# Kernel optimization log

Measured on AMD Instinct MI355X. Metric: run time of the kernel, lower is better.

## Reference

```python
import jax, jax.numpy as jnp
import numpy as np

C = 64   # in_planes
F = 40   # n_freq
T = 512  # n_frame
B = 16


def setup_inputs() -> dict:
    key = jax.random.key(0)
    kx, kq, kk, kv = jax.random.split(key, 4)
    x = jax.random.normal(kx, (B, C, F, T), dtype=jnp.float32)
    # 1x1 conv weights, no bias: [out_ch, in_ch]
    s = 1.0 / np.sqrt(C)
    Wq = jax.random.uniform(kq, (C, C), dtype=jnp.float32, minval=-s, maxval=s)
    Wk = jax.random.uniform(kk, (C, C), dtype=jnp.float32, minval=-s, maxval=s)
    Wv = jax.random.uniform(kv, (C, C), dtype=jnp.float32, minval=-s, maxval=s)
    return {"x": x, "Wq": Wq, "Wk": Wk, "Wv": Wv}


def _proj_tokens(W, x):
    # 1x1 conv (channel mix) then permute(0,3,2,1) + view -> [B, T, F*C]
    y = jnp.einsum('oc,bcft->btfo', W, x)      # [B, T, F, C]
    b, t, f, c = y.shape
    return y.reshape(b, t, f * c)


def reference(x, Wq, Wk, Wv):
    n_batch, n_planes, n_freq, n_frame = x.shape
    d = n_freq * n_planes
    q = _proj_tokens(Wq, x)                     # [B, T, d]
    k = _proj_tokens(Wk, x)
    v = _proj_tokens(Wv, x)
    scores = jnp.einsum('bqd,bkd->bqk', q, k) / jnp.sqrt(jnp.float32(d))
    attn = jax.nn.softmax(scores, axis=-1)      # [B, T, T]
    out = jnp.einsum('bqk,bkd->bqd', attn, v)   # [B, T, d]
    out = out.reshape(n_batch, n_frame, n_freq, n_planes)
    return jnp.transpose(out, (0, 3, 2, 1))     # [B, C, F, T]
```

## Files before the change

### kernel.cpp

```cpp
#include <hip/hip_runtime.h>

constexpr int B_ = 16, C_ = 64, F_ = 40, T_ = 512;
constexpr int D_ = F_ * C_;
constexpr float SCALE = 0.019764235376052372f;

typedef __attribute__((ext_vector_type(8))) short s16x8;
typedef __attribute__((ext_vector_type(4))) short s16x4;
typedef __attribute__((ext_vector_type(4))) float f32x4;

static __device__ __forceinline__ short f2bf(float f) {
  union { float f; unsigned u; } v; v.f = f;
  unsigned r = v.u + 0x7fffu + ((v.u >> 16) & 1u);
  return (short)(r >> 16);
}

static __device__ __forceinline__ f32x4 mfma16(s16x8 a, s16x8 b, f32x4 c) {
  return __builtin_amdgcn_mfma_f32_16x16x32_bf16(a, b, c, 0, 0, 0);
}

static __device__ __forceinline__ void gl2lds16(const short* g, short* l) {
  __builtin_amdgcn_global_load_lds(
      (const __attribute__((address_space(1))) unsigned int*)g,
      (__attribute__((address_space(3))) unsigned int*)l, 16, 0, 0);
}

__global__ __launch_bounds__(256) void wcvt_kernel(
    const float* __restrict__ Wq, const float* __restrict__ Wk,
    const float* __restrict__ Wv, short* __restrict__ Wb,
    float* __restrict__ rowsum)
{
  const int n = blockIdx.x * 256 + threadIdx.x;
  const int p = n >> 9;
  const int r = n & 511;
  const int mi = r >> 7;
  const int ks = (r >> 6) & 1;
  const int lane = r & 63;
  const int o = mi * 16 + (lane & 15);
  const int cb = ks * 32 + (lane >> 4) * 8;
  const float* src = (p == 0) ? Wq : (p == 1) ? Wk : Wv;
  const float sc = (p == 0) ? SCALE : 1.0f;
  const float4 a = *(const float4*)(src + o * 64 + cb);
  const float4 b2 = *(const float4*)(src + o * 64 + cb + 4);
  s16x8 s;
  s[0] = f2bf(a.x * sc);  s[1] = f2bf(a.y * sc);
  s[2] = f2bf(a.z * sc);  s[3] = f2bf(a.w * sc);
  s[4] = f2bf(b2.x * sc); s[5] = f2bf(b2.y * sc);
  s[6] = f2bf(b2.z * sc); s[7] = f2bf(b2.w * sc);
  *(s16x8*)&Wb[n * 8] = s;

  for (int i = n; i < B_ * T_; i += 6 * 256) rowsum[i] = 0.0f;
}

__global__ __launch_bounds__(256, 2) void proj_kernel(
    const float* __restrict__ x, const short* __restrict__ Wb,
    short* __restrict__ Q, short* __restrict__ K, short* __restrict__ V)
{
  constexpr int XS = 132;
  __shared__ __align__(16) short Xl[64 * XS];
  char* Ost = (char*)Xl;

  const int b = blockIdx.z, f = blockIdx.y, tt = blockIdx.x;
  const int tid = threadIdx.x;

  const float* xp = x + (((size_t)b * 64) * 40 + f) * 512 + tt * 128;
  #pragma unroll
  for (int it = 0; it < 8; ++it) {
    const int i = tid + it * 256;
    const int c = i >> 5, j = i & 31;
    const float4 v4 = *(const float4*)(xp + (size_t)c * (F_ * T_) + j * 4);
    s16x4 s4; s4[0] = f2bf(v4.x); s4[1] = f2bf(v4.y);
    s4[2] = f2bf(v4.z); s4[3] = f2bf(v4.w);
    *(s16x4*)&Xl[c * XS + j * 4] = s4;
  }
  __syncthreads();

  const int w = tid >> 6, lane = tid & 63;
  const int quad = lane >> 4, c16 = lane & 15;
  const int tl = w * 32;

  s16x8 bfrag[2][2];
  #pragma unroll
  for (int ni = 0; ni < 2; ++ni)
    #pragma unroll
    for (int ks = 0; ks < 2; ++ks) {
      const int t = tl + ni * 16 + c16;
      const int cb = ks * 32 + quad * 8;
      s16x8 tmp;
      #pragma unroll
      for (int j = 0; j < 8; ++j) tmp[j] = Xl[(cb + j) * XS + t];
      bfrag[ni][ks] = tmp;
    }
  __syncthreads();

  #pragma unroll
  for (int p = 0; p < 3; ++p) {
    s16x8 wfrag[4][2];
    #pragma unroll
    for (int mi = 0; mi < 4; ++mi)
      #pragma unroll
      for (int ks = 0; ks < 2; ++ks)
        wfrag[mi][ks] = *(const s16x8*)(Wb + ((p * 8 + mi * 2 + ks) * 64 + lane) * 8);

    if (p < 2) {
      f32x4 acc[4][2] = {};
      #pragma unroll
      for (int ks = 0; ks < 2; ++ks)
        #pragma unroll
        for (int mi = 0; mi < 4; ++mi)
          #pragma unroll
          for (int ni = 0; ni < 2; ++ni)
            acc[mi][ni] = mfma16(wfrag[mi][ks], bfrag[ni][ks], acc[mi][ni]);
      __syncthreads();
      #pragma unroll
      for (int mi = 0; mi < 4; ++mi)
        #pragma unroll
        for (int ni = 0; ni < 2; ++ni) {
          const int trow = tl + ni * 16 + c16;
          unsigned addr = trow * 128 + (mi * 32 + quad * 8);
          addr ^= (unsigned)((trow & 7) << 4);
          s16x4 s4;
          #pragma unroll
          for (int r = 0; r < 4; ++r) s4[r] = f2bf(acc[mi][ni][r]);
          *(s16x4*)(Ost + addr) = s4;
        }
      __syncthreads();
      short* outp = (p == 0) ? Q : K;
      #pragma unroll
      for (int pass = 0; pass < 4; ++pass) {
        const int row = pass * 32 + (tid >> 3);
        const int s16off = tid & 7;
        unsigned a2 = row * 128 + s16off * 16;
        a2 ^= (unsigned)((row & 7) << 4);
        const s16x8 vz = *(const s16x8*)(Ost + a2);
        *(s16x8*)&outp[(size_t)(b * 512 + tt * 128 + row) * D_ + f * 64 + s16off * 8] = vz;
      }
    } else {
      f32x4 acc[2][4] = {};
      #pragma unroll
      for (int ks = 0; ks < 2; ++ks)
        #pragma unroll
        for (int ni = 0; ni < 2; ++ni)
          #pragma unroll
          for (int mi = 0; mi < 4; ++mi)
            acc[ni][mi] = mfma16(bfrag[ni][ks], wfrag[mi][ks], acc[ni][mi]);
      __syncthreads();
      #pragma unroll
      for (int ni = 0; ni < 2; ++ni)
        #pragma unroll
        for (int mi = 0; mi < 4; ++mi) {
          const int orow = mi * 16 + c16;
          unsigned addr = orow * 256 + (tl + ni * 16 + quad * 4) * 2;
          addr ^= (unsigned)((orow & 7) << 4);
          s16x4 s4;
          #pragma unroll
          for (int r = 0; r < 4; ++r) s4[r] = f2bf(acc[ni][mi][r]);
          *(s16x4*)(Ost + addr) = s4;
        }
      __syncthreads();
      #pragma unroll
      for (int pass = 0; pass < 4; ++pass) {
        const int row = pass * 16 + (tid >> 4);
        const int s16off = tid & 15;
        unsigned a2 = row * 256 + s16off * 16;
        a2 ^= (unsigned)((row & 7) << 4);
        const s16x8 vz = *(const s16x8*)(Ost + a2);
        *(s16x8*)&V[((size_t)(b * D_ + f * 64 + row)) * 512 + tt * 128 + s16off * 8] = vz;
      }
    }
    if (p < 2) __syncthreads();
  }
}

__global__ __launch_bounds__(256) void scores_kernel(
    const short* __restrict__ Q, const short* __restrict__ K,
    short* __restrict__ A, float* __restrict__ rowsum)
{
  __shared__ __align__(16) short As[64 * 64];
  __shared__ __align__(16) short Bs[128 * 64];
  const int b = blockIdx.y;
  const int mt = blockIdx.x >> 2, nt = blockIdx.x & 3;
  const int m0 = mt * 64, n0 = nt * 128;
  const int tid = threadIdx.x;
  const int w = tid >> 6, lane = tid & 63, quad = lane >> 4, c16 = lane & 15;
  const int wm = (w >> 1) * 32, wn = (w & 1) * 64;

  const short* qb = Q + (size_t)(b * 512 + m0) * D_;
  const short* kb = K + (size_t)(b * 512 + n0) * D_;

  const short* agp[2];
  short* aldsb[2];
  #pragma unroll
  for (int i = 0; i < 2; ++i) {
    const int s = i * 256 + tid, row = s >> 3;
    const int g = (s & 7) ^ (row & 7);
    agp[i] = qb + (size_t)row * D_ + g * 8;
    aldsb[i] = &As[(i * 256 + w * 64) * 8];
  }
  const short* bgp[4];
  short* bldsb[4];
  #pragma unroll
  for (int i = 0; i < 4; ++i) {
    const int s = i * 256 + tid, row = s >> 3;
    const int g = (s & 7) ^ (row & 7);
    bgp[i] = kb + (size_t)row * D_ + g * 8;
    bldsb[i] = &Bs[(i * 256 + w * 64) * 8];
  }

  const short* amp[2][2];
  #pragma unroll
  for (int mi = 0; mi < 2; ++mi)
    #pragma unroll
    for (int ks = 0; ks < 2; ++ks) {
      const int row = wm + mi * 16 + c16;
      const int g = (ks * 4 + quad) ^ (row & 7);
      amp[mi][ks] = &As[row * 64 + g * 8];
    }
  const short* bmp[4][2];
  #pragma unroll
  for (int ni = 0; ni < 4; ++ni)
    #pragma unroll
    for (int ks = 0; ks < 2; ++ks) {
      const int row = wn + ni * 16 + c16;
      const int g = (ks * 4 + quad) ^ (row & 7);
      bmp[ni][ks] = &Bs[row * 64 + g * 8];
    }

  f32x4 acc[2][4] = {};
  constexpr int NK = D_ / 64;
  for (int kk = 0; kk < NK; ++kk) {
    const int ko = kk * 64;
    __syncthreads();
    #pragma unroll
    for (int i = 0; i < 2; ++i) gl2lds16(agp[i] + ko, aldsb[i]);
    #pragma unroll
    for (int i = 0; i < 4; ++i) gl2lds16(bgp[i] + ko, bldsb[i]);
    __syncthreads();
    s16x8 am[2][2], bm[4][2];
    #pragma unroll
    for (int mi = 0; mi < 2; ++mi)
      #pragma unroll
      for (int ks = 0; ks < 2; ++ks) am[mi][ks] = *(const s16x8*)amp[mi][ks];
    #pragma unroll
    for (int ni = 0; ni < 4; ++ni)
      #pragma unroll
      for (int ks = 0; ks < 2; ++ks) bm[ni][ks] = *(const s16x8*)bmp[ni][ks];
    #pragma unroll
    for (int ks = 0; ks < 2; ++ks)
      #pragma unroll
      for (int mi = 0; mi < 2; ++mi)
        #pragma unroll
        for (int ni = 0; ni < 4; ++ni)
          acc[mi][ni] = mfma16(am[mi][ks], bm[ni][ks], acc[mi][ni]);
  }

  float* rsb = rowsum + b * 512;
  #pragma unroll
  for (int mi = 0; mi < 2; ++mi)
    #pragma unroll
    for (int r = 0; r < 4; ++r) {
      float part = 0.f;
      #pragma unroll
      for (int ni = 0; ni < 4; ++ni) {
        const float e0 = __expf(acc[mi][ni][r]);
        acc[mi][ni][r] = e0;
        part += e0;
      }
      #pragma unroll
      for (int mask = 1; mask < 16; mask <<= 1) part += __shfl_xor(part, mask);
      if (c16 == 0)
        atomicAdd(&rsb[m0 + wm + mi * 16 + quad * 4 + r], part);
    }

  short* ap = A + ((size_t)b * 512) * 512;
  #pragma unroll
  for (int mi = 0; mi < 2; ++mi)
    #pragma unroll
    for (int ni = 0; ni < 4; ++ni) {
      const int kcol = n0 + wn + ni * 16 + c16;
      const int qr = m0 + wm + mi * 16 + quad * 4;
      #pragma unroll
      for (int r = 0; r < 4; ++r)
        ap[(size_t)(qr + r) * 512 + kcol] = f2bf(acc[mi][ni][r]);
    }
}

__global__ __launch_bounds__(256) void pv_kernel(
    const short* __restrict__ A, const short* __restrict__ V,
    const float* __restrict__ rowsum, float* __restrict__ out)
{
  __shared__ __align__(16) short As[128 * 64];
  __shared__ __align__(16) short Bs[128 * 64];
  const int b = blockIdx.y;
  const int mt = blockIdx.x / 20, dt = blockIdx.x % 20;
  const int m0 = mt * 128, n0 = dt * 128;
  const int tid = threadIdx.x;
  const int w = tid >> 6, lane = tid & 63, quad = lane >> 4, c16 = lane & 15;
  const int wm = (w >> 1) * 64, wn = (w & 1) * 64;

  const short* ab = A + ((size_t)b * 512 + m0) * 512;
  const short* vb = V + ((size_t)b * D_ + n0) * 512;

  const short* agp[4]; short* aldsb[4];
  const short* bgp[4]; short* bldsb[4];
  #pragma unroll
  for (int i = 0; i < 4; ++i) {
    const int s = i * 256 + tid, row = s >> 3;
    const int g = (s & 7) ^ (row & 7);
    agp[i] = ab + (size_t)row * 512 + g * 8;
    bgp[i] = vb + (size_t)row * 512 + g * 8;
    aldsb[i] = &As[(i * 256 + w * 64) * 8];
    bldsb[i] = &Bs[(i * 256 + w * 64) * 8];
  }

  const short* amp[4][2];
  const short* bmp[4][2];
  #pragma unroll
  for (int mi = 0; mi < 4; ++mi)
    #pragma unroll
    for (int ks = 0; ks < 2; ++ks) {
      const int rowa = wm + mi * 16 + c16;
      const int rowb = wn + mi * 16 + c16;
      amp[mi][ks] = &As[rowa * 64 + (((ks * 4 + quad) ^ (rowa & 7)) * 8)];
      bmp[mi][ks] = &Bs[rowb * 64 + (((ks * 4 + quad) ^ (rowb & 7)) * 8)];
    }

  f32x4 acc[4][4] = {};
  constexpr int NK = 512 / 64;
  for (int kk = 0; kk < NK; ++kk) {
    const int ko = kk * 64;
    __syncthreads();
    #pragma unroll
    for (int i = 0; i < 4; ++i) gl2lds16(agp[i] + ko, aldsb[i]);
    #pragma unroll
    for (int i = 0; i < 4; ++i) gl2lds16(bgp[i] + ko, bldsb[i]);
    __syncthreads();
    s16x8 am[4][2], bm[4][2];
    #pragma unroll
    for (int mi = 0; mi < 4; ++mi)
      #pragma unroll
      for (int ks = 0; ks < 2; ++ks) {
        am[mi][ks] = *(const s16x8*)amp[mi][ks];
        bm[mi][ks] = *(const s16x8*)bmp[mi][ks];
      }
    #pragma unroll
    for (int ks = 0; ks < 2; ++ks)
      #pragma unroll
      for (int mi = 0; mi < 4; ++mi)
        #pragma unroll
        for (int ni = 0; ni < 4; ++ni)
          acc[mi][ni] = mfma16(am[mi][ks], bm[ni][ks], acc[mi][ni]);
  }

  const float* rsb = rowsum + b * 512;
  #pragma unroll
  for (int mi = 0; mi < 4; ++mi) {
    const int t = m0 + wm + mi * 16 + quad * 4;
    const float4 rs = *(const float4*)(rsb + t);
    const float i0 = 1.0f / rs.x, i1 = 1.0f / rs.y;
    const float i2 = 1.0f / rs.z, i3 = 1.0f / rs.w;
    #pragma unroll
    for (int ni = 0; ni < 4; ++ni) {
      acc[mi][ni][0] *= i0; acc[mi][ni][1] *= i1;
      acc[mi][ni][2] *= i2; acc[mi][ni][3] *= i3;
    }
  }

  #pragma unroll
  for (int mi = 0; mi < 4; ++mi)
    #pragma unroll
    for (int ni = 0; ni < 4; ++ni) {
      const int d = n0 + wn + ni * 16 + c16;
      const int ff = d >> 6, cc = d & 63;
      const int t = m0 + wm + mi * 16 + quad * 4;
      float4 o4;
      o4.x = acc[mi][ni][0]; o4.y = acc[mi][ni][1];
      o4.z = acc[mi][ni][2]; o4.w = acc[mi][ni][3];
      *(float4*)&out[(((size_t)b * 64 + cc) * 40 + ff) * 512 + t] = o4;
    }
}

extern "C" void kernel_launch(void* const* d_in, const int* in_sizes, int n_in,
                              void* d_out, int out_size, void* d_ws, size_t ws_size,
                              hipStream_t stream)
{
  const float* x  = (const float*)d_in[0];
  const float* Wq = (const float*)d_in[1];
  const float* Wk = (const float*)d_in[2];
  const float* Wv = (const float*)d_in[3];
  float* out = (float*)d_out;

  char* ws = (char*)d_ws;
  constexpr size_t QB = (size_t)B_ * T_ * D_ * 2;
  constexpr size_t AB = (size_t)B_ * T_ * T_ * 2;
  short* Q  = (short*)(ws);
  short* Kt = (short*)(ws + QB);
  short* Vt = (short*)(ws + 2 * QB);
  short* At = (short*)(ws + 3 * QB);
  short* Wb = (short*)(ws + 3 * QB + AB);
  float* rowsum = (float*)(ws + 3 * QB + AB + 24576);

  wcvt_kernel<<<dim3(6), 256, 0, stream>>>(Wq, Wk, Wv, Wb, rowsum);
  proj_kernel<<<dim3(4, 40, 16), 256, 0, stream>>>(x, Wb, Q, Kt, Vt);
  scores_kernel<<<dim3(32, 16), 256, 0, stream>>>(Q, Kt, At, rowsum);
  pv_kernel<<<dim3(80, 16), 256, 0, stream>>>(At, Vt, rowsum, out);
}
```

Before: 248.3 us.

## Store Q, K, V and attention matrix in contiguous 128x64 tile-blocked layout

Reorganizes the intermediate Q, K, V and probability buffers into tile-blocked layouts where each 128-row by 64-column block is contiguous (8192 elements). The projection, scores and PV kernels now write and read these blocks, so each K-step global-to-LDS load reads one contiguous 16 KB chunk instead of rows strided by D or 512. This targets DRAM/TLB locality and coalescing of the tile loads, at the cost of more complex indexing that must match exactly across all three kernels.

```diff
diff --git a/kernel.cpp b/kernel.cpp
--- a/kernel.cpp
+++ b/kernel.cpp
@@ -3,6 +3,7 @@
 constexpr int B_ = 16, C_ = 64, F_ = 40, T_ = 512;
 constexpr int D_ = F_ * C_;
 constexpr float SCALE = 0.019764235376052372f;
+
 
 typedef __attribute__((ext_vector_type(8))) short s16x8;
 typedef __attribute__((ext_vector_type(4))) short s16x4;
@@ -124,7 +125,7 @@
           *(s16x4*)(Ost + addr) = s4;
         }
       __syncthreads();
-      short* outp = (p == 0) ? Q : K;
+      short* tb = ((p == 0) ? Q : K) + ((size_t)((b * 4 + tt) * 40 + f)) * 8192;
       #pragma unroll
       for (int pass = 0; pass < 4; ++pass) {
         const int row = pass * 32 + (tid >> 3);
@@ -132,7 +133,7 @@
         unsigned a2 = row * 128 + s16off * 16;
         a2 ^= (unsigned)((row & 7) << 4);
         const s16x8 vz = *(const s16x8*)(Ost + a2);
-        *(s16x8*)&outp[(size_t)(b * 512 + tt * 128 + row) * D_ + f * 64 + s16off * 8] = vz;
+        *(s16x8*)&tb[row * 64 + s16off * 8] = vz;
       }
     } else {
       f32x4 acc[2][4] = {};
@@ -157,6 +158,8 @@
           *(s16x4*)(Ost + addr) = s4;
         }
       __syncthreads();
+      const size_t vbase = (((size_t)(b * 20 + (f >> 1)) * 8) + tt * 2) * 8192
+                         + (size_t)((f & 1) * 64) * 64;
       #pragma unroll
       for (int pass = 0; pass < 4; ++pass) {
         const int row = pass * 16 + (tid >> 4);
@@ -164,7 +167,9 @@
         unsigned a2 = row * 256 + s16off * 16;
         a2 ^= (unsigned)((row & 7) << 4);
         const s16x8 vz = *(const s16x8*)(Ost + a2);
-        *(s16x8*)&V[((size_t)(b * D_ + f * 64 + row)) * 512 + tt * 128 + s16off * 8] = vz;
+        const int h = s16off >> 3;
+        const int tg = s16off & 7;
+        *(s16x8*)&V[vbase + (size_t)h * 8192 + row * 64 + tg * 8] = vz;
       }
     }
     if (p < 2) __syncthreads();
@@ -184,25 +189,24 @@
   const int w = tid >> 6, lane = tid & 63, quad = lane >> 4, c16 = lane & 15;
   const int wm = (w >> 1) * 32, wn = (w & 1) * 64;
 
-  const short* qb = Q + (size_t)(b * 512 + m0) * D_;
-  const short* kb = K + (size_t)(b * 512 + n0) * D_;
-
-  const short* agp[2];
-  short* aldsb[2];
+  const short* qb = Q + ((size_t)((b * 4 + (mt >> 1)) * 40)) * 8192
+                      + (size_t)((mt & 1) * 64) * 64;
+  const short* kb = K + ((size_t)((b * 4 + nt) * 40)) * 8192;
+
+  const short* agp[2]; short* aldsb[2];
   #pragma unroll
   for (int i = 0; i < 2; ++i) {
     const int s = i * 256 + tid, row = s >> 3;
     const int g = (s & 7) ^ (row & 7);
-    agp[i] = qb + (size_t)row * D_ + g * 8;
+    agp[i] = qb + row * 64 + g * 8;
     aldsb[i] = &As[(i * 256 + w * 64) * 8];
   }
-  const short* bgp[4];
-  short* bldsb[4];
+  const short* bgp[4]; short* bldsb[4];
   #pragma unroll
   for (int i = 0; i < 4; ++i) {
     const int s = i * 256 + tid, row = s >> 3;
     const int g = (s & 7) ^ (row & 7);
-    bgp[i] = kb + (size_t)row * D_ + g * 8;
+    bgp[i] = kb + row * 64 + g * 8;
     bldsb[i] = &Bs[(i * 256 + w * 64) * 8];
   }
 
@@ -228,7 +232,7 @@
   f32x4 acc[2][4] = {};
   constexpr int NK = D_ / 64;
   for (int kk = 0; kk < NK; ++kk) {
-    const int ko = kk * 64;
+    const size_t ko = (size_t)kk * 8192;
     __syncthreads();
     #pragma unroll
     for (int i = 0; i < 2; ++i) gl2lds16(agp[i] + ko, aldsb[i]);
@@ -271,16 +275,18 @@
         atomicAdd(&rsb[m0 + wm + mi * 16 + quad * 4 + r], part);
     }
 
-  short* ap = A + ((size_t)b * 512) * 512;
+  short* ap = A + ((size_t)(b * 4 + (mt >> 1)) * 8) * 8192
+                + (size_t)((mt & 1) * 64) * 64;
+  const int ktb = nt * 2 + (wn >> 6);
   #pragma unroll
   for (int mi = 0; mi < 2; ++mi)
     #pragma unroll
     for (int ni = 0; ni < 4; ++ni) {
-      const int kcol = n0 + wn + ni * 16 + c16;
-      const int qr = m0 + wm + mi * 16 + quad * 4;
+      const int kc = ni * 16 + c16;
+      const int mr = wm + mi * 16 + quad * 4;
       #pragma unroll
       for (int r = 0; r < 4; ++r)
-        ap[(size_t)(qr + r) * 512 + kcol] = f2bf(acc[mi][ni][r]);
+        ap[(size_t)ktb * 8192 + (mr + r) * 64 + kc] = f2bf(acc[mi][ni][r]);
     }
 }
 
@@ -297,8 +303,8 @@
   const int w = tid >> 6, lane = tid & 63, quad = lane >> 4, c16 = lane & 15;
   const int wm = (w >> 1) * 64, wn = (w & 1) * 64;
 
-  const short* ab = A + ((size_t)b * 512 + m0) * 512;
-  const short* vb = V + ((size_t)b * D_ + n0) * 512;
+  const short* ab = A + ((size_t)(b * 4 + mt) * 8) * 8192;
+  const short* vb = V + ((size_t)(b * 20 + dt) * 8) * 8192;
 
   const short* agp[4]; short* aldsb[4];
   const short* bgp[4]; short* bldsb[4];
@@ -306,8 +312,8 @@
   for (int i = 0; i < 4; ++i) {
     const int s = i * 256 + tid, row = s >> 3;
     const int g = (s & 7) ^ (row & 7);
-    agp[i] = ab + (size_t)row * 512 + g * 8;
-    bgp[i] = vb + (size_t)row * 512 + g * 8;
+    agp[i] = ab + row * 64 + g * 8;
+    bgp[i] = vb + row * 64 + g * 8;
     aldsb[i] = &As[(i * 256 + w * 64) * 8];
     bldsb[i] = &Bs[(i * 256 + w * 64) * 8];
   }
@@ -327,7 +333,7 @@
   f32x4 acc[4][4] = {};
   constexpr int NK = 512 / 64;
   for (int kk = 0; kk < NK; ++kk) {
-    const int ko = kk * 64;
+    const size_t ko = (size_t)kk * 8192;
     __syncthreads();
     #pragma unroll
     for (int i = 0; i < 4; ++i) gl2lds16(agp[i] + ko, aldsb[i]);
```

Result: no change. 248.1 us (-0.1%).
